# Optimization experiments

Hardware: AMD Instinct MI355X
Metric: run time of the kernel (lower is better)

Reference implementation:

```python
import jax, jax.numpy as jnp
import numpy as np

N_NODES = 50000
N_EDGES = 800000
HID = 64
HEADS = 4


def setup_inputs() -> dict:
    key = jax.random.key(0)
    ks = jax.random.split(key, 8)
    x = jax.random.normal(ks[0], (N_NODES, HID), dtype=jnp.float32)
    edge_index = jax.random.randint(ks[1], (2, N_EDGES), 0, N_NODES, dtype=jnp.int32)
    W_gat = jax.random.normal(ks[2], (HID, HEADS * HID), dtype=jnp.float32) * 0.1
    att_src = jax.random.normal(ks[3], (HEADS, HID), dtype=jnp.float32) * 0.1
    att_dst = jax.random.normal(ks[4], (HEADS, HID), dtype=jnp.float32) * 0.1
    bias_gat = jnp.zeros((HEADS * HID,), dtype=jnp.float32)
    W_lin = jax.random.normal(ks[5], (HEADS * HID, HID), dtype=jnp.float32) * 0.06
    b_lin = jnp.zeros((HID,), dtype=jnp.float32)
    return {"x": x, "edge_index": edge_index, "W_gat": W_gat, "att_src": att_src,
            "att_dst": att_dst, "bias_gat": bias_gat, "W_lin": W_lin, "b_lin": b_lin}


def reference(x, edge_index, W_gat, att_src, att_dst, bias_gat, W_lin, b_lin):
    N = x.shape[0]
    H, C = HEADS, HID
    # PyG GATConv default: add self-loops
    loops = jnp.arange(N, dtype=edge_index.dtype)
    ei = jnp.concatenate([edge_index, jnp.stack([loops, loops])], axis=1)
    src, dst = ei[0], ei[1]  # messages flow src -> dst; softmax grouped by dst

    h = (x @ W_gat).reshape(N, H, C)                     # [N,H,C]
    a_src = jnp.einsum('nhc,hc->nh', h, att_src)          # [N,H]
    a_dst = jnp.einsum('nhc,hc->nh', h, att_dst)          # [N,H]

    alpha = jax.nn.leaky_relu(a_src[src] + a_dst[dst], negative_slope=0.2)  # [E,H]
    amax = jax.ops.segment_max(alpha, dst, num_segments=N)
    amax = jnp.where(jnp.isfinite(amax), amax, 0.0)
    ex = jnp.exp(alpha - amax[dst])
    denom = jax.ops.segment_sum(ex, dst, num_segments=N)
    coef = ex / (denom[dst] + 1e-16)                      # [E,H] attention weights

    msg = h[src] * coef[:, :, None]                       # [E,H,C]
    out = jax.ops.segment_sum(msg, dst, num_segments=N)   # [N,H,C]
    out = out.reshape(N, H * C) + bias_gat                # concat heads + bias

    out = jax.nn.elu(out)                                 # ELU
    return out @ W_lin + b_lin                            # final Linear
```

## Files before the change

### kernel.cpp

```cpp
#include <hip/hip_runtime.h>

#define HIDc 64
#define HEADSc 4
#define HCc 256

typedef unsigned short ushort_t;
typedef unsigned int uint_t;
typedef __attribute__((ext_vector_type(8))) short bf16x8;
typedef __attribute__((ext_vector_type(4))) float f32x4;

__device__ inline ushort_t f2bf(float f) {
    uint_t u = __float_as_uint(f);
    u += 0x7FFFu + ((u >> 16) & 1u);
    return (ushort_t)(u >> 16);
}
__device__ inline float bfu(uint_t lo16) { return __uint_as_float(lo16 << 16); }
__device__ inline float lrelu(float a) { return a > 0.f ? a : 0.2f * a; }
__device__ inline float elu(float o)  { return o > 0.f ? o : (__expf(o) - 1.f); }

__global__ __launch_bounds__(256) void k0_prep(
    const float* __restrict__ Wg, const float* __restrict__ Wl,
    ushort_t* __restrict__ WgT, ushort_t* __restrict__ WlT)
{
    int i = blockIdx.x * 256 + threadIdx.x;
    if (i < 64 * 256) {
        int k = i >> 8, n = i & 255;
        WgT[n * 64 + k] = f2bf(Wg[i]);
    } else {
        int j = i - 64 * 256;
        int k = j >> 6, n = j & 63;
        WlT[n * 256 + k] = f2bf(Wl[j]);
    }
}

__global__ __launch_bounds__(256) void k1_mfma(
    const float* __restrict__ x, const ushort_t* __restrict__ WgT,
    ushort_t* __restrict__ h, int N)
{
    const int w = threadIdx.x >> 6, l = threadIdx.x & 63;
    const int lr = l & 15, ko = l >> 4;
    const int base = blockIdx.x * 32;
    const int colb = w * 64;

    bf16x8 afr[2][2];
#pragma unroll
    for (int mt = 0; mt < 2; ++mt) {
        int row = base + mt * 16 + lr;
        int rowc = row < N ? row : N - 1;
        const float* xr = x + (size_t)rowc * HIDc + ko * 8;
#pragma unroll
        for (int kb = 0; kb < 2; ++kb) {
            float t0[8];
            *(float4*)t0       = *(const float4*)(xr + kb * 32);
            *(float4*)(t0 + 4) = *(const float4*)(xr + kb * 32 + 4);
            bf16x8 a;
#pragma unroll
            for (int j = 0; j < 8; ++j) a[j] = (short)f2bf(t0[j]);
            afr[mt][kb] = a;
        }
    }

    f32x4 acc[2][4];
#pragma unroll
    for (int mt = 0; mt < 2; ++mt)
#pragma unroll
        for (int nt = 0; nt < 4; ++nt) acc[mt][nt] = (f32x4)0.f;

#pragma unroll
    for (int nt = 0; nt < 4; ++nt) {
        const int col = colb + nt * 16 + lr;
        const ushort_t* wr = WgT + col * HIDc + ko * 8;
        bf16x8 b0 = *(const bf16x8*)wr;
        bf16x8 b1 = *(const bf16x8*)(wr + 32);
#pragma unroll
        for (int mt = 0; mt < 2; ++mt) {
            acc[mt][nt] = __builtin_amdgcn_mfma_f32_16x16x32_bf16(
                afr[mt][0], b0, acc[mt][nt], 0, 0, 0);
            acc[mt][nt] = __builtin_amdgcn_mfma_f32_16x16x32_bf16(
                afr[mt][1], b1, acc[mt][nt], 0, 0, 0);
        }
    }

#pragma unroll
    for (int mt = 0; mt < 2; ++mt)
#pragma unroll
        for (int r = 0; r < 4; ++r) {
            int row = base + mt * 16 + ko * 4 + r;
            if (row < N) {
#pragma unroll
                for (int nt = 0; nt < 4; ++nt)
                    h[(size_t)row * HCc + colb + nt * 16 + lr] =
                        f2bf(acc[mt][nt][r]);
            }
        }
}

__global__ __launch_bounds__(256) void k1b_attn(
    const uint2* __restrict__ h2, const float4* __restrict__ as4,
    const float4* __restrict__ ad4, float* __restrict__ a_src,
    float* __restrict__ a_dst, int N)
{
    const int wid = threadIdx.x >> 6, l = threadIdx.x & 63;
    const int n = blockIdx.x * 4 + wid;
    if (n >= N) return;
    const uint2 v = h2[(size_t)n * 64 + l];
    const float4 a = as4[l];
    const float4 d = ad4[l];
    const float h0 = bfu(v.x & 0xFFFFu), h1 = bfu(v.x >> 16);
    const float h2v = bfu(v.y & 0xFFFFu), h3 = bfu(v.y >> 16);
    float ps = h0 * a.x + h1 * a.y + h2v * a.z + h3 * a.w;
    float pd = h0 * d.x + h1 * d.y + h2v * d.z + h3 * d.w;
#pragma unroll
    for (int o = 1; o < 16; o <<= 1) {
        ps += __shfl_xor(ps, o, 64);
        pd += __shfl_xor(pd, o, 64);
    }
    if ((l & 15) == 0) {
        a_src[n * HEADSc + (l >> 4)] = ps;
        a_dst[n * HEADSc + (l >> 4)] = pd;
    }
}

__global__ void k2_count(const int* __restrict__ ei, int* __restrict__ counts,
                         int E, int N)
{
    int i = blockIdx.x * blockDim.x + threadIdx.x;
    int total = E + N;
    if (i < total) {
        int d = (i < E) ? ei[E + i] : (i - E);
        atomicAdd(&counts[d], 1);
    }
}

__global__ __launch_bounds__(256) void k2_scanA(
    const int* __restrict__ counts, int* __restrict__ bsum, int N)
{
    const int b = blockIdx.x, t = threadIdx.x;
    const int i0 = b * 1024 + t * 4;
    int s = 0;
    if (i0 + 3 < N) {
        int4 v = *(const int4*)(counts + i0);
        s = v.x + v.y + v.z + v.w;
    } else {
        for (int k = 0; k < 4; ++k) if (i0 + k < N) s += counts[i0 + k];
    }
    const int lane = t & 63, wid = t >> 6;
#pragma unroll
    for (int o = 1; o < 64; o <<= 1) s += __shfl_xor(s, o, 64);
    __shared__ int ws[4];
    if (lane == 0) ws[wid] = s;
    __syncthreads();
    if (t == 0) bsum[b] = ws[0] + ws[1] + ws[2] + ws[3];
}

__global__ __launch_bounds__(64) void k2_scanB(
    const int* __restrict__ bsum, int* __restrict__ boff, int NB,
    int* __restrict__ offsets, int N)
{
    const int t = threadIdx.x;
    int carry = 0;
    for (int base = 0; base < NB; base += 64) {
        int v = (base + t < NB) ? bsum[base + t] : 0;
        int incl = v;
#pragma unroll
        for (int o = 1; o < 64; o <<= 1) {
            int u = __shfl_up(incl, o, 64);
            if (t >= o) incl += u;
        }
        if (base + t < NB) boff[base + t] = carry + incl - v;
        carry += __shfl(incl, 63, 64);
    }
    if (t == 0) offsets[N] = carry;
}

__global__ __launch_bounds__(256) void k2_scanC(
    const int* __restrict__ counts, const int* __restrict__ boff,
    int* __restrict__ offsets, int* __restrict__ cursor, int N)
{
    const int b = blockIdx.x, t = threadIdx.x;
    const int i0 = b * 1024 + t * 4;
    int c0 = 0, c1 = 0, c2 = 0, c3 = 0;
    if (i0 + 3 < N) {
        int4 v = *(const int4*)(counts + i0);
        c0 = v.x; c1 = v.y; c2 = v.z; c3 = v.w;
    } else {
        if (i0     < N) c0 = counts[i0];
        if (i0 + 1 < N) c1 = counts[i0 + 1];
        if (i0 + 2 < N) c2 = counts[i0 + 2];
        if (i0 + 3 < N) c3 = counts[i0 + 3];
    }
    const int s4 = c0 + c1 + c2 + c3;
    const int lane = t & 63, wid = t >> 6;
    int incl = s4;
#pragma unroll
    for (int o = 1; o < 64; o <<= 1) {
        int u = __shfl_up(incl, o, 64);
        if (lane >= o) incl += u;
    }
    __shared__ int ws[4];
    if (lane == 63) ws[wid] = incl;
    __syncthreads();
    int woff = 0;
    for (int w = 0; w < wid; ++w) woff += ws[w];
    const int pref = boff[b] + woff + incl - s4;
    const int o0 = pref, o1 = pref + c0, o2 = o1 + c1, o3 = o2 + c2;
    if (i0 + 3 < N) {
        *(int4*)(offsets + i0) = make_int4(o0, o1, o2, o3);
        *(int4*)(cursor  + i0) = make_int4(o0, o1, o2, o3);
    } else {
        if (i0     < N) { offsets[i0]     = o0; cursor[i0]     = o0; }
        if (i0 + 1 < N) { offsets[i0 + 1] = o1; cursor[i0 + 1] = o1; }
        if (i0 + 2 < N) { offsets[i0 + 2] = o2; cursor[i0 + 2] = o2; }
        if (i0 + 3 < N) { offsets[i0 + 3] = o3; cursor[i0 + 3] = o3; }
    }
}

__global__ void k2_fill(const int* __restrict__ ei, int* __restrict__ cursor,
                        int* __restrict__ csr_src, int E, int N)
{
    int i = blockIdx.x * blockDim.x + threadIdx.x;
    int total = E + N;
    if (i < total) {
        int s, d;
        if (i < E) { s = ei[i]; d = ei[E + i]; }
        else       { s = d = i - E; }
        int pos = atomicAdd(&cursor[d], 1);
        csr_src[pos] = s;
    }
}

__global__ __launch_bounds__(256) void k3_aggregate(
    const uint2* __restrict__ h2,
    const float4* __restrict__ a_src4,
    const float4* __restrict__ a_dst4,
    const int* __restrict__ offsets, const int* __restrict__ csr_src,
    const float4* __restrict__ bias4,
    uint2* __restrict__ act2, int N)
{
    __shared__ float s_p[HEADSc][64 * 4];
    __shared__ int   s_src[HEADSc][64];

    const int wid = threadIdx.x >> 6, lane = threadIdx.x & 63;
    const int n = blockIdx.x * 4 + wid;
    if (n >= N) return;

    const int beg = offsets[n], end = offsets[n + 1];
    const float4 adst = a_dst4[n];
    const int head = lane >> 4, sub = lane & 15;
    const uint_t cix = (uint_t)(head * 16 + sub);

    float acc0 = 0.f, acc1 = 0.f, acc2 = 0.f, acc3 = 0.f;
    float den = 0.f;

    float* pw = s_p[wid];
    int*   sw = s_src[wid];

    for (int cb = beg; cb < end; cb += 64) {
        const int cnt = min(64, end - cb);
        const int sn = (lane < cnt) ? csr_src[cb + lane] : 0;
        const float4 as = a_src4[sn];
        float p0 = __expf(lrelu(as.x + adst.x));
        float p1 = __expf(lrelu(as.y + adst.y));
        float p2 = __expf(lrelu(as.z + adst.z));
        float p3 = __expf(lrelu(as.w + adst.w));
        ((float4*)pw)[lane] = make_float4(p0, p1, p2, p3);
        sw[lane] = sn;

        float accc0 = 0.f, accc1 = 0.f, accc2 = 0.f, accc3 = 0.f;
#pragma unroll 4
        for (int e = 0; e < cnt; ++e) {
            const int   sv = sw[e];
            const float pe = pw[e * 4 + head];
            den += pe;
            const uint2 v = h2[(uint_t)sv * 64u + cix];
            accc0 += pe * __uint_as_float(v.x << 16);
            accc1 += pe * __uint_as_float(v.x & 0xFFFF0000u);
            accc2 += pe * __uint_as_float(v.y << 16);
            accc3 += pe * __uint_as_float(v.y & 0xFFFF0000u);
        }
        acc0 += accc0; acc1 += accc1; acc2 += accc2; acc3 += accc3;
    }

    const float r = 1.f / (den + 1e-16f);
    const float4 b = bias4[cix];
    const float o0 = elu(acc0 * r + b.x);
    const float o1 = elu(acc1 * r + b.y);
    const float o2 = elu(acc2 * r + b.z);
    const float o3 = elu(acc3 * r + b.w);
    uint2 ov;
    ov.x = (uint_t)f2bf(o0) | ((uint_t)f2bf(o1) << 16);
    ov.y = (uint_t)f2bf(o2) | ((uint_t)f2bf(o3) << 16);
    act2[(uint_t)n * 64u + cix] = ov;
}

__global__ __launch_bounds__(256) void k4_mfma(
    const ushort_t* __restrict__ act, const ushort_t* __restrict__ WlT,
    const float* __restrict__ bl, float* __restrict__ out, int N)
{
    const int w = threadIdx.x >> 6, l = threadIdx.x & 63;
    const int lr = l & 15, ko = l >> 4;
    const int base = blockIdx.x * 64 + w * 16;

    f32x4 acc[4];
#pragma unroll
    for (int nt = 0; nt < 4; ++nt) acc[nt] = (f32x4)0.f;

    int row = base + lr;
    int rowc = row < N ? row : N - 1;
    const ushort_t* ar = act + (size_t)rowc * HCc + ko * 8;

#pragma unroll
    for (int kb = 0; kb < 8; ++kb) {
        bf16x8 a = *(const bf16x8*)(ar + kb * 32);
#pragma unroll
        for (int nt = 0; nt < 4; ++nt) {
            const int col = nt * 16 + lr;
            bf16x8 b = *(const bf16x8*)(WlT + col * HCc + kb * 32 + ko * 8);
            acc[nt] = __builtin_amdgcn_mfma_f32_16x16x32_bf16(a, b, acc[nt], 0, 0, 0);
        }
    }

#pragma unroll
    for (int r = 0; r < 4; ++r) {
        int orow = base + ko * 4 + r;
        if (orow < N) {
#pragma unroll
            for (int nt = 0; nt < 4; ++nt)
                out[(size_t)orow * HIDc + nt * 16 + lr] = acc[nt][r] + bl[nt * 16 + lr];
        }
    }
}

extern "C" void kernel_launch(void* const* d_in, const int* in_sizes, int n_in,
                              void* d_out, int out_size, void* d_ws, size_t ws_size,
                              hipStream_t stream)
{
    const float* x       = (const float*)d_in[0];
    const int*   ei      = (const int*)  d_in[1];
    const float* Wg      = (const float*)d_in[2];
    const float* att_src = (const float*)d_in[3];
    const float* att_dst = (const float*)d_in[4];
    const float* bias_g  = (const float*)d_in[5];
    const float* Wl      = (const float*)d_in[6];
    const float* bl      = (const float*)d_in[7];
    float* out = (float*)d_out;

    const int N = in_sizes[0] / HIDc;
    const int E = in_sizes[1] / 2;
    const int total = E + N;
    const int NB = (N + 1023) / 1024;

    char* w = (char*)d_ws;
    size_t off = 0;
    auto carve = [&](size_t bytes) {
        void* p = w + off;
        off = (off + bytes + 255) & ~(size_t)255;
        return p;
    };
    ushort_t* h     = (ushort_t*)carve((size_t)N * HCc * 2);
    ushort_t* act   = (ushort_t*)carve((size_t)N * HCc * 2);
    float* a_src    = (float*)carve((size_t)N * HEADSc * 4);
    float* a_dst    = (float*)carve((size_t)N * HEADSc * 4);
    int*   counts   = (int*)  carve((size_t)N * 4);
    int*   offsets  = (int*)  carve((size_t)(N + 1) * 4);
    int*   cursor   = (int*)  carve((size_t)N * 4);
    int*   csr_src  = (int*)  carve((size_t)total * 4);
    int*   bsum     = (int*)  carve((size_t)NB * 4);
    int*   boff     = (int*)  carve((size_t)NB * 4);
    ushort_t* WgT   = (ushort_t*)carve((size_t)HIDc * HCc * 2);
    ushort_t* WlT   = (ushort_t*)carve((size_t)HCc * HIDc * 2);
    (void)ws_size;

    hipMemsetAsync(counts, 0, (size_t)N * 4, stream);

    k0_prep<<<128, 256, 0, stream>>>(Wg, Wl, WgT, WlT);
    k1_mfma<<<(N + 31) / 32, 256, 0, stream>>>(x, WgT, h, N);
    k1b_attn<<<(N + 3) / 4, 256, 0, stream>>>(
        (const uint2*)h, (const float4*)att_src, (const float4*)att_dst,
        a_src, a_dst, N);
    k2_count<<<(total + 255) / 256, 256, 0, stream>>>(ei, counts, E, N);
    k2_scanA<<<NB, 256, 0, stream>>>(counts, bsum, N);
    k2_scanB<<<1, 64, 0, stream>>>(bsum, boff, NB, offsets, N);
    k2_scanC<<<NB, 256, 0, stream>>>(counts, boff, offsets, cursor, N);
    k2_fill<<<(total + 255) / 256, 256, 0, stream>>>(ei, cursor, csr_src, E, N);
    k3_aggregate<<<(N + 3) / 4, 256, 0, stream>>>(
        (const uint2*)h, (const float4*)a_src, (const float4*)a_dst,
        offsets, csr_src, (const float4*)bias_g, (uint2*)act, N);
    k4_mfma<<<(N + 63) / 64, 256, 0, stream>>>(act, WlT, bl, out, N);
}
```

Measured before the change: 286.2 us.

## Fuse attention logits into GEMM, vectorize CSR build, widen aggregation loads

Several unrelated changes ship together. The attention-score kernel is folded into the first MFMA GEMM, which now stages h through shared memory so it can write coalesced rows and compute a_src/a_dst without re-reading h. The CSR build stops issuing atomics for self-loops: their slots are reserved during the scan and filled at each segment's last position. The count and fill kernels use int4 loads with four atomics per thread. The aggregation kernel handles two edges per iteration, with each half-wave loading 16-byte h chunks, and reduces the halves with a cross-lane shuffle, trading extra LDS and register use for fewer launches and wider memory transactions.

```diff
diff --git a/kernel.cpp b/kernel.cpp
--- a/kernel.cpp
+++ b/kernel.cpp
@@ -15,6 +15,8 @@
     return (ushort_t)(u >> 16);
 }
 __device__ inline float bfu(uint_t lo16) { return __uint_as_float(lo16 << 16); }
+__device__ inline float bflo(uint_t u) { return __uint_as_float(u << 16); }
+__device__ inline float bfhi(uint_t u) { return __uint_as_float(u & 0xFFFF0000u); }
 __device__ inline float lrelu(float a) { return a > 0.f ? a : 0.2f * a; }
 __device__ inline float elu(float o)  { return o > 0.f ? o : (__expf(o) - 1.f); }
 
@@ -35,9 +37,14 @@
 
 __global__ __launch_bounds__(256) void k1_mfma(
     const float* __restrict__ x, const ushort_t* __restrict__ WgT,
-    ushort_t* __restrict__ h, int N)
-{
-    const int w = threadIdx.x >> 6, l = threadIdx.x & 63;
+    const float* __restrict__ att_src, const float* __restrict__ att_dst,
+    ushort_t* __restrict__ h, float* __restrict__ a_src, float* __restrict__ a_dst,
+    int N)
+{
+    __shared__ ushort_t hs[32][264];
+
+    const int t = threadIdx.x;
+    const int w = t >> 6, l = t & 63;
     const int lr = l & 15, ko = l >> 4;
     const int base = blockIdx.x * 32;
     const int colb = w * 64;
@@ -84,51 +91,51 @@
 #pragma unroll
     for (int mt = 0; mt < 2; ++mt)
 #pragma unroll
-        for (int r = 0; r < 4; ++r) {
-            int row = base + mt * 16 + ko * 4 + r;
-            if (row < N) {
-#pragma unroll
-                for (int nt = 0; nt < 4; ++nt)
-                    h[(size_t)row * HCc + colb + nt * 16 + lr] =
-                        f2bf(acc[mt][nt][r]);
-            }
-        }
-}
-
-__global__ __launch_bounds__(256) void k1b_attn(
-    const uint2* __restrict__ h2, const float4* __restrict__ as4,
-    const float4* __restrict__ ad4, float* __restrict__ a_src,
-    float* __restrict__ a_dst, int N)
-{
-    const int wid = threadIdx.x >> 6, l = threadIdx.x & 63;
-    const int n = blockIdx.x * 4 + wid;
-    if (n >= N) return;
-    const uint2 v = h2[(size_t)n * 64 + l];
-    const float4 a = as4[l];
-    const float4 d = ad4[l];
-    const float h0 = bfu(v.x & 0xFFFFu), h1 = bfu(v.x >> 16);
-    const float h2v = bfu(v.y & 0xFFFFu), h3 = bfu(v.y >> 16);
-    float ps = h0 * a.x + h1 * a.y + h2v * a.z + h3 * a.w;
-    float pd = h0 * d.x + h1 * d.y + h2v * d.z + h3 * d.w;
-#pragma unroll
-    for (int o = 1; o < 16; o <<= 1) {
-        ps += __shfl_xor(ps, o, 64);
-        pd += __shfl_xor(pd, o, 64);
-    }
-    if ((l & 15) == 0) {
-        a_src[n * HEADSc + (l >> 4)] = ps;
-        a_dst[n * HEADSc + (l >> 4)] = pd;
-    }
-}
-
-__global__ void k2_count(const int* __restrict__ ei, int* __restrict__ counts,
-                         int E, int N)
-{
-    int i = blockIdx.x * blockDim.x + threadIdx.x;
-    int total = E + N;
-    if (i < total) {
-        int d = (i < E) ? ei[E + i] : (i - E);
-        atomicAdd(&counts[d], 1);
+        for (int r = 0; r < 4; ++r)
+#pragma unroll
+            for (int nt = 0; nt < 4; ++nt)
+                hs[mt * 16 + ko * 4 + r][colb + nt * 16 + lr] =
+                    f2bf(acc[mt][nt][r]);
+    __syncthreads();
+
+    for (int rr = w; rr < 32; rr += 4) {
+        int gn = base + rr;
+        if (gn < N) {
+            uint2 v = *(const uint2*)&hs[rr][l * 4];
+            *(uint2*)&h[(size_t)gn * HCc + l * 4] = v;
+        }
+    }
+
+    const int node = t >> 3, hd = (t >> 1) & 3, half = t & 1;
+    const int gn2 = base + node;
+    const int cb2 = hd * 64 + half * 32;
+    float ps = 0.f, pd = 0.f;
+#pragma unroll
+    for (int j = 0; j < 32; ++j) {
+        float hv = bfu((uint_t)hs[node][cb2 + j]);
+        ps += hv * att_src[cb2 + j];
+        pd += hv * att_dst[cb2 + j];
+    }
+    ps += __shfl_xor(ps, 1, 64);
+    pd += __shfl_xor(pd, 1, 64);
+    if (half == 0 && gn2 < N) {
+        a_src[gn2 * HEADSc + hd] = ps;
+        a_dst[gn2 * HEADSc + hd] = pd;
+    }
+}
+
+__global__ void k2_count(const int* __restrict__ dst, int* __restrict__ counts,
+                         int E)
+{
+    int i = (blockIdx.x * blockDim.x + threadIdx.x) * 4;
+    if (i + 3 < E) {
+        int4 d = *(const int4*)(dst + i);
+        atomicAdd(&counts[d.x], 1);
+        atomicAdd(&counts[d.y], 1);
+        atomicAdd(&counts[d.z], 1);
+        atomicAdd(&counts[d.w], 1);
+    } else {
+        for (int k = i; k < E; ++k) atomicAdd(&counts[dst[k]], 1);
     }
 }
 
@@ -140,9 +147,9 @@
     int s = 0;
     if (i0 + 3 < N) {
         int4 v = *(const int4*)(counts + i0);
-        s = v.x + v.y + v.z + v.w;
-    } else {
-        for (int k = 0; k < 4; ++k) if (i0 + k < N) s += counts[i0 + k];
+        s = v.x + v.y + v.z + v.w + 4;
+    } else {
+        for (int k = 0; k < 4; ++k) if (i0 + k < N) s += counts[i0 + k] + 1;
     }
     const int lane = t & 63, wid = t >> 6;
 #pragma unroll
@@ -179,7 +186,7 @@
 {
     const int b = blockIdx.x, t = threadIdx.x;
     const int i0 = b * 1024 + t * 4;
-    int c0 = 0, c1 = 0, c2 = 0, c3 = 0;
+    int c0 = -1, c1 = -1, c2 = -1, c3 = -1;
     if (i0 + 3 < N) {
         int4 v = *(const int4*)(counts + i0);
         c0 = v.x; c1 = v.y; c2 = v.z; c3 = v.w;
@@ -189,7 +196,9 @@
         if (i0 + 2 < N) c2 = counts[i0 + 2];
         if (i0 + 3 < N) c3 = counts[i0 + 3];
     }
-    const int s4 = c0 + c1 + c2 + c3;
+    const int w0 = c0 >= 0 ? c0 + 1 : 0, w1 = c1 >= 0 ? c1 + 1 : 0;
+    const int w2 = c2 >= 0 ? c2 + 1 : 0, w3 = c3 >= 0 ? c3 + 1 : 0;
+    const int s4 = w0 + w1 + w2 + w3;
     const int lane = t & 63, wid = t >> 6;
     int incl = s4;
 #pragma unroll
@@ -201,41 +210,54 @@
     if (lane == 63) ws[wid] = incl;
     __syncthreads();
     int woff = 0;
-    for (int w = 0; w < wid; ++w) woff += ws[w];
+    for (int q = 0; q < wid; ++q) woff += ws[q];
     const int pref = boff[b] + woff + incl - s4;
-    const int o0 = pref, o1 = pref + c0, o2 = o1 + c1, o3 = o2 + c2;
+    const int o0 = pref, o1 = o0 + w0, o2 = o1 + w1, o3 = o2 + w2;
     if (i0 + 3 < N) {
         *(int4*)(offsets + i0) = make_int4(o0, o1, o2, o3);
         *(int4*)(cursor  + i0) = make_int4(o0, o1, o2, o3);
     } else {
-        if (i0     < N) { offsets[i0]     = o0; cursor[i0]     = o0; }
-        if (i0 + 1 < N) { offsets[i0 + 1] = o1; cursor[i0 + 1] = o1; }
-        if (i0 + 2 < N) { offsets[i0 + 2] = o2; cursor[i0 + 2] = o2; }
-        if (i0 + 3 < N) { offsets[i0 + 3] = o3; cursor[i0 + 3] = o3; }
-    }
-}
-
-__global__ void k2_fill(const int* __restrict__ ei, int* __restrict__ cursor,
-                        int* __restrict__ csr_src, int E, int N)
-{
-    int i = blockIdx.x * blockDim.x + threadIdx.x;
-    int total = E + N;
-    if (i < total) {
-        int s, d;
-        if (i < E) { s = ei[i]; d = ei[E + i]; }
-        else       { s = d = i - E; }
-        int pos = atomicAdd(&cursor[d], 1);
-        csr_src[pos] = s;
+        if (c0 >= 0) { offsets[i0]     = o0; cursor[i0]     = o0; }
+        if (c1 >= 0) { offsets[i0 + 1] = o1; cursor[i0 + 1] = o1; }
+        if (c2 >= 0) { offsets[i0 + 2] = o2; cursor[i0 + 2] = o2; }
+        if (c3 >= 0) { offsets[i0 + 3] = o3; cursor[i0 + 3] = o3; }
+    }
+}
+
+__global__ void k2_fill(const int* __restrict__ ei, const int* __restrict__ offsets,
+                        int* __restrict__ cursor, int* __restrict__ csr_src,
+                        int E, int N, int EB4)
+{
+    int gid = blockIdx.x * blockDim.x + threadIdx.x;
+    if (gid < EB4) {
+        int i = gid * 4;
+        if (i + 3 < E) {
+            int4 s4 = *(const int4*)(ei + i);
+            int4 d4 = *(const int4*)(ei + E + i);
+            int p;
+            p = atomicAdd(&cursor[d4.x], 1); csr_src[p] = s4.x;
+            p = atomicAdd(&cursor[d4.y], 1); csr_src[p] = s4.y;
+            p = atomicAdd(&cursor[d4.z], 1); csr_src[p] = s4.z;
+            p = atomicAdd(&cursor[d4.w], 1); csr_src[p] = s4.w;
+        } else {
+            for (int k = i; k < E; ++k) {
+                int p = atomicAdd(&cursor[ei[E + k]], 1);
+                csr_src[p] = ei[k];
+            }
+        }
+    } else {
+        int n = gid - EB4;
+        if (n < N) csr_src[offsets[n + 1] - 1] = n;
     }
 }
 
 __global__ __launch_bounds__(256) void k3_aggregate(
-    const uint2* __restrict__ h2,
+    const uint4* __restrict__ h4,
     const float4* __restrict__ a_src4,
     const float4* __restrict__ a_dst4,
     const int* __restrict__ offsets, const int* __restrict__ csr_src,
     const float4* __restrict__ bias4,
-    uint2* __restrict__ act2, int N)
+    uint4* __restrict__ act4, int N)
 {
     __shared__ float s_p[HEADSc][64 * 4];
     __shared__ int   s_src[HEADSc][64];
@@ -246,10 +268,10 @@
 
     const int beg = offsets[n], end = offsets[n + 1];
     const float4 adst = a_dst4[n];
-    const int head = lane >> 4, sub = lane & 15;
-    const uint_t cix = (uint_t)(head * 16 + sub);
-
-    float acc0 = 0.f, acc1 = 0.f, acc2 = 0.f, acc3 = 0.f;
+    const int eh = lane >> 5, li = lane & 31;
+    const int head = li >> 3;
+
+    float acc[8] = {0.f, 0.f, 0.f, 0.f, 0.f, 0.f, 0.f, 0.f};
     float den = 0.f;
 
     float* pw = s_p[wid];
@@ -257,40 +279,52 @@
 
     for (int cb = beg; cb < end; cb += 64) {
         const int cnt = min(64, end - cb);
-        const int sn = (lane < cnt) ? csr_src[cb + lane] : 0;
+        const bool valid = lane < cnt;
+        const int sn = valid ? csr_src[cb + lane] : 0;
         const float4 as = a_src4[sn];
-        float p0 = __expf(lrelu(as.x + adst.x));
-        float p1 = __expf(lrelu(as.y + adst.y));
-        float p2 = __expf(lrelu(as.z + adst.z));
-        float p3 = __expf(lrelu(as.w + adst.w));
+        float p0 = valid ? __expf(lrelu(as.x + adst.x)) : 0.f;
+        float p1 = valid ? __expf(lrelu(as.y + adst.y)) : 0.f;
+        float p2 = valid ? __expf(lrelu(as.z + adst.z)) : 0.f;
+        float p3 = valid ? __expf(lrelu(as.w + adst.w)) : 0.f;
         ((float4*)pw)[lane] = make_float4(p0, p1, p2, p3);
         sw[lane] = sn;
 
-        float accc0 = 0.f, accc1 = 0.f, accc2 = 0.f, accc3 = 0.f;
-#pragma unroll 4
-        for (int e = 0; e < cnt; ++e) {
+#pragma unroll 2
+        for (int e2 = 0; e2 < cnt; e2 += 2) {
+            const int   e  = e2 + eh;
             const int   sv = sw[e];
             const float pe = pw[e * 4 + head];
             den += pe;
-            const uint2 v = h2[(uint_t)sv * 64u + cix];
-            accc0 += pe * __uint_as_float(v.x << 16);
-            accc1 += pe * __uint_as_float(v.x & 0xFFFF0000u);
-            accc2 += pe * __uint_as_float(v.y << 16);
-            accc3 += pe * __uint_as_float(v.y & 0xFFFF0000u);
-        }
-        acc0 += accc0; acc1 += accc1; acc2 += accc2; acc3 += accc3;
-    }
-
-    const float r = 1.f / (den + 1e-16f);
-    const float4 b = bias4[cix];
-    const float o0 = elu(acc0 * r + b.x);
-    const float o1 = elu(acc1 * r + b.y);
-    const float o2 = elu(acc2 * r + b.z);
-    const float o3 = elu(acc3 * r + b.w);
-    uint2 ov;
-    ov.x = (uint_t)f2bf(o0) | ((uint_t)f2bf(o1) << 16);
-    ov.y = (uint_t)f2bf(o2) | ((uint_t)f2bf(o3) << 16);
-    act2[(uint_t)n * 64u + cix] = ov;
+            const uint4 v = h4[(uint_t)sv * 32u + li];
+            acc[0] += pe * bflo(v.x); acc[1] += pe * bfhi(v.x);
+            acc[2] += pe * bflo(v.y); acc[3] += pe * bfhi(v.y);
+            acc[4] += pe * bflo(v.z); acc[5] += pe * bfhi(v.z);
+            acc[6] += pe * bflo(v.w); acc[7] += pe * bfhi(v.w);
+        }
+    }
+
+#pragma unroll
+    for (int q = 0; q < 8; ++q) acc[q] += __shfl_xor(acc[q], 32, 64);
+    den += __shfl_xor(den, 32, 64);
+
+    if (eh == 0) {
+        const float r = 1.f / (den + 1e-16f);
+        const float4 b0 = bias4[li * 2], b1 = bias4[li * 2 + 1];
+        const float o0 = elu(acc[0] * r + b0.x);
+        const float o1 = elu(acc[1] * r + b0.y);
+        const float o2 = elu(acc[2] * r + b0.z);
+        const float o3 = elu(acc[3] * r + b0.w);
+        const float o4 = elu(acc[4] * r + b1.x);
+        const float o5 = elu(acc[5] * r + b1.y);
+        const float o6 = elu(acc[6] * r + b1.z);
+        const float o7 = elu(acc[7] * r + b1.w);
+        uint4 ov;
+        ov.x = (uint_t)f2bf(o0) | ((uint_t)f2bf(o1) << 16);
+        ov.y = (uint_t)f2bf(o2) | ((uint_t)f2bf(o3) << 16);
+        ov.z = (uint_t)f2bf(o4) | ((uint_t)f2bf(o5) << 16);
+        ov.w = (uint_t)f2bf(o6) | ((uint_t)f2bf(o7) << 16);
+        act4[(uint_t)n * 32u + li] = ov;
+    }
 }
 
 __global__ __launch_bounds__(256) void k4_mfma(
@@ -347,8 +381,8 @@
 
     const int N = in_sizes[0] / HIDc;
     const int E = in_sizes[1] / 2;
-    const int total = E + N;
     const int NB = (N + 1023) / 1024;
+    const int EB4 = (E + 3) / 4;
 
     char* w = (char*)d_ws;
     size_t off = 0;
@@ -364,27 +398,26 @@
     int*   counts   = (int*)  carve((size_t)N * 4);
     int*   offsets  = (int*)  carve((size_t)(N + 1) * 4);
     int*   cursor   = (int*)  carve((size_t)N * 4);
-    int*   csr_src  = (int*)  carve((size_t)total * 4);
+    int*   csr_src  = (int*)  carve((size_t)(E + N) * 4);
     int*   bsum     = (int*)  carve((size_t)NB * 4);
     int*   boff     = (int*)  carve((size_t)NB * 4);
     ushort_t* WgT   = (ushort_t*)carve((size_t)HIDc * HCc * 2);
     ushort_t* WlT   = (ushort_t*)carve((size_t)HCc * HIDc * 2);
-    (void)ws_size;
+    (void)ws_size; (void)n_in; (void)out_size;
 
     hipMemsetAsync(counts, 0, (size_t)N * 4, stream);
 
     k0_prep<<<128, 256, 0, stream>>>(Wg, Wl, WgT, WlT);
-    k1_mfma<<<(N + 31) / 32, 256, 0, stream>>>(x, WgT, h, N);
-    k1b_attn<<<(N + 3) / 4, 256, 0, stream>>>(
-        (const uint2*)h, (const float4*)att_src, (const float4*)att_dst,
-        a_src, a_dst, N);
-    k2_count<<<(total + 255) / 256, 256, 0, stream>>>(ei, counts, E, N);
+    k1_mfma<<<(N + 31) / 32, 256, 0, stream>>>(x, WgT, att_src, att_dst,
+                                               h, a_src, a_dst, N);
+    k2_count<<<(EB4 + 255) / 256, 256, 0, stream>>>(ei + E, counts, E);
     k2_scanA<<<NB, 256, 0, stream>>>(counts, bsum, N);
     k2_scanB<<<1, 64, 0, stream>>>(bsum, boff, NB, offsets, N);
     k2_scanC<<<NB, 256, 0, stream>>>(counts, boff, offsets, cursor, N);
-    k2_fill<<<(total + 255) / 256, 256, 0, stream>>>(ei, cursor, csr_src, E, N);
+    k2_fill<<<(EB4 + N + 255) / 256, 256, 0, stream>>>(ei, offsets, cursor,
+                                                       csr_src, E, N, EB4);
     k3_aggregate<<<(N + 3) / 4, 256, 0, stream>>>(
-        (const uint2*)h, (const float4*)a_src, (const float4*)a_dst,
-        offsets, csr_src, (const float4*)bias_g, (uint2*)act, N);
+        (const uint4*)h, (const float4*)a_src, (const float4*)a_dst,
+        offsets, csr_src, (const float4*)bias_g, (uint4*)act, N);
     k4_mfma<<<(N + 63) / 64, 256, 0, stream>>>(act, WlT, bl, out, N);
 }
```

Result: no change. 288.2 us (+0.7%).
